# Optimization experiments

Hardware: AMD Instinct MI355X
Metric: run time of the kernel (lower is better)

## Reference

```python
import jax, jax.numpy as jnp
import numpy as np

EPS = 1e-5

def _layernorm(x, w, b):
    mu = jnp.mean(x, axis=-1, keepdims=True)
    var = jnp.var(x, axis=-1, keepdims=True)
    return (x - mu) * jax.lax.rsqrt(var + EPS) * w + b

def setup_inputs() -> dict:
    key = jax.random.key(0)
    ks = jax.random.split(key, 9)
    b, s, dim = 4, 4096, 2048
    m, n, dim_ctx = 8, 64, 1024
    heads, dim_head = 8, 64
    inner = heads * dim_head
    x = jax.random.normal(ks[0], (b, s, dim), dtype=jnp.float32)
    context = jax.random.normal(ks[1], (b, m, n, dim_ctx), dtype=jnp.float32)
    media_locations = jax.random.randint(ks[2], (b, s), 0, m, dtype=jnp.int64)
    scale = 0.02
    norm_w = jnp.ones((dim,), jnp.float32)
    norm_b = jnp.zeros((dim,), jnp.float32)
    normc_w = jnp.ones((dim_ctx,), jnp.float32)
    normc_b = jnp.zeros((dim_ctx,), jnp.float32)
    Wq = jax.random.normal(ks[3], (dim, inner), jnp.float32) * scale
    Wkv = jax.random.normal(ks[4], (dim_ctx, 2 * inner), jnp.float32) * scale
    Wout = jax.random.normal(ks[5], (inner, dim), jnp.float32) * scale
    return {"x": x, "context": context, "media_locations": media_locations,
            "norm_w": norm_w, "norm_b": norm_b, "normc_w": normc_w, "normc_b": normc_b,
            "Wq": Wq, "Wkv": Wkv, "Wout": Wout}

def reference(x, context, media_locations, norm_w, norm_b, normc_w, normc_b, Wq, Wkv, Wout):
    heads, dim_head = 8, 64
    b, m, n, dc = context.shape
    scale = dim_head ** -0.5
    xn = _layernorm(x, norm_w, norm_b)                       # [b,s,dim]
    ctx = _layernorm(context.reshape(b, m * n, dc), normc_w, normc_b)  # [b,mn,dc]
    q = xn @ Wq                                              # [b,s,inner]
    kv = ctx @ Wkv                                           # [b,mn,2*inner]
    k, v = jnp.split(kv, 2, axis=-1)
    def to_heads(t):
        return t.reshape(t.shape[0], t.shape[1], heads, dim_head).transpose(0, 2, 1, 3)
    q, k, v = to_heads(q), to_heads(k), to_heads(v)          # [b,h,*,d]
    sim = jnp.einsum('bhid,bhjd->bhij', q, k) * scale        # [b,h,s,mn]
    # image-causal mask: kv token j belongs to image j//n; query i may only
    # attend to image media_locations[b,i] (negative index => all masked)
    j_img = jnp.arange(m * n) // n                           # [mn]
    allowed = (media_locations[:, :, None] == j_img[None, None, :]) & (media_locations[:, :, None] >= 0)
    sim = jnp.where(allowed[:, None, :, :], sim, -jnp.inf)
    attn = jax.nn.softmax(sim, axis=-1)
    out = jnp.einsum('bhij,bhjd->bhid', attn, v)             # [b,h,s,d]
    out = out.transpose(0, 2, 1, 3).reshape(b, x.shape[1], heads * dim_head)
    return out @ Wout
```

## Files before the change

### kernel.cpp

```cpp
#include <hip/hip_runtime.h>

typedef unsigned short u16;
typedef unsigned int u32;
typedef __attribute__((ext_vector_type(8))) short short8;
typedef __attribute__((ext_vector_type(4))) short short4_t;
typedef __attribute__((ext_vector_type(4))) float f32x4;

__device__ __forceinline__ float bf2f(u16 u){ return __uint_as_float(((u32)u)<<16); }
__device__ __forceinline__ u16 f2bf(float f){ u32 x = __float_as_uint(f); return (u16)((x + 0x7FFFu + ((x>>16)&1u)) >> 16); }

#define OFF_FLAG   ((size_t)0)
#define OFF_COUNTS ((size_t)256)
#define OFF_LISTS  ((size_t)4096)
#define OFF_XN     ((size_t)(1<<20))
#define OFF_CTXN   (OFF_XN    + (size_t)67108864)
#define OFF_WQT    (OFF_CTXN  + (size_t)4194304)
#define OFF_WKVT   (OFF_WQT   + (size_t)2097152)
#define OFF_WOUTT  (OFF_WKVT  + (size_t)2097152)
#define OFF_Q      (OFF_WOUTT + (size_t)2097152)
#define OFF_KV     (OFF_Q     + (size_t)16777216)
#define OFF_ATTN   (OFF_KV    + (size_t)4194304)
#define OFF_VT     (OFF_ATTN  + (size_t)16777216)
#define WS_NEEDED  (OFF_VT    + (size_t)2097152)

__global__ __launch_bounds__(256) void prep_all(const float* __restrict__ x, const float* __restrict__ nw,
                                                const float* __restrict__ nb, u16* __restrict__ xn,
                                                const float* __restrict__ ctx, const float* __restrict__ ncw,
                                                const float* __restrict__ ncb, u16* __restrict__ ctxn,
                                                const float* __restrict__ Wq, const float* __restrict__ Wkv,
                                                const float* __restrict__ Wout, u16* __restrict__ WqT,
                                                u16* __restrict__ WkvT, u16* __restrict__ WoutT,
                                                const int* __restrict__ ml32, int* __restrict__ flag,
                                                int* __restrict__ counts){
  int id = blockIdx.x, tid = threadIdx.x;
  __shared__ float red[8];
  __shared__ float t[32][33];
  __shared__ int nz;
  if (id < 16384){
    constexpr int D = 2048, VEC = 8;
    const float* xr = x + (size_t)id*D;
    float v[VEC];
    #pragma unroll
    for (int i=0;i<VEC;i+=4){
      f32x4 f = *(const f32x4*)(xr + tid*VEC + i);
      v[i]=f[0]; v[i+1]=f[1]; v[i+2]=f[2]; v[i+3]=f[3];
    }
    float s=0.f, sq=0.f;
    #pragma unroll
    for (int i=0;i<VEC;++i){ s += v[i]; sq += v[i]*v[i]; }
    #pragma unroll
    for (int off=32;off;off>>=1){ s += __shfl_xor(s,off,64); sq += __shfl_xor(sq,off,64); }
    int lane = tid&63, wid = tid>>6;
    if (lane==0){ red[wid]=s; red[4+wid]=sq; }
    __syncthreads();
    s  = red[0]+red[1]+red[2]+red[3];
    sq = red[4]+red[5]+red[6]+red[7];
    float mu = s/(float)D;
    float var = sq/(float)D - mu*mu;
    float rs = rsqrtf(var + 1e-5f);
    u16 o[VEC];
    #pragma unroll
    for (int i=0;i<VEC;i+=4){
      f32x4 wv = *(const f32x4*)(nw + tid*VEC + i);
      f32x4 bv = *(const f32x4*)(nb + tid*VEC + i);
      #pragma unroll
      for (int u=0;u<4;++u) o[i+u] = f2bf((v[i+u]-mu)*rs*wv[u] + bv[u]);
    }
    *(short8*)(xn + (size_t)id*D + tid*8) = *(short8*)o;
  } else if (id < 18432){
    constexpr int D = 1024;
    int row = id - 16384;
    const float* xr = ctx + (size_t)row*D;
    f32x4 f = *(const f32x4*)(xr + tid*4);
    float s = f[0]+f[1]+f[2]+f[3];
    float sq = f[0]*f[0]+f[1]*f[1]+f[2]*f[2]+f[3]*f[3];
    #pragma unroll
    for (int off=32;off;off>>=1){ s += __shfl_xor(s,off,64); sq += __shfl_xor(sq,off,64); }
    int lane = tid&63, wid = tid>>6;
    if (lane==0){ red[wid]=s; red[4+wid]=sq; }
    __syncthreads();
    s  = red[0]+red[1]+red[2]+red[3];
    sq = red[4]+red[5]+red[6]+red[7];
    float mu = s/(float)D;
    float var = sq/(float)D - mu*mu;
    float rs = rsqrtf(var + 1e-5f);
    f32x4 wv = *(const f32x4*)(ncw + tid*4);
    f32x4 bv = *(const f32x4*)(ncb + tid*4);
    u16 o[4];
    #pragma unroll
    for (int u=0;u<4;++u) o[u] = f2bf((f[u]-mu)*rs*wv[u] + bv[u]);
    *(short4_t*)(ctxn + (size_t)row*D + tid*4) = *(short4_t*)o;
  } else if (id < 21504){
    int wid2 = id - 18432;
    const float* in; u16* out; int K, N, tile, tx_n;
    if (wid2 < 1024)      { in=Wq;   out=WqT;   K=2048; N=512;  tile=wid2;      tx_n=16; }
    else if (wid2 < 2048) { in=Wkv;  out=WkvT;  K=1024; N=1024; tile=wid2-1024; tx_n=32; }
    else                  { in=Wout; out=WoutT; K=512;  N=2048; tile=wid2-2048; tx_n=64; }
    int n0 = (tile % tx_n)*32, k0 = (tile / tx_n)*32;
    int tx = tid & 31, ty = tid >> 5;
    #pragma unroll
    for (int r=0;r<32;r+=8) t[ty+r][tx] = in[(size_t)(k0+ty+r)*N + n0+tx];
    __syncthreads();
    #pragma unroll
    for (int r=0;r<32;r+=8) out[(size_t)(n0+ty+r)*K + k0+tx] = f2bf(t[tx][ty+r]);
  } else {
    if (tid < 32) counts[tid] = 0;
    if (tid == 0) nz = 0;
    __syncthreads();
    if (tid < 128 && ml32[2*tid+1] != 0) atomicAdd(&nz, 1);
    __syncthreads();
    if (tid == 0) flag[0] = (nz == 0) ? 1 : 0;
  }
}

template<int MODE>
__device__ __forceinline__ void gemm_body(u16 (*lds)[2][128*32],
                                          const u16* __restrict__ A, const u16* __restrict__ B,
                                          void* __restrict__ Cv, int M, int N, int K, int wg0, int nwg,
                                          u16* __restrict__ vtp){
  int tid = threadIdx.x, lane = tid&63, wid = tid>>6;
  int nbn = N>>7;
  int wg = wg0;
  int cpx = nwg>>3;
  wg = (wg&7)*cpx + (wg>>3);
  int brow = wg/nbn, bcol = wg%nbn;

  auto stage = [&](int buf, int kt){
    #pragma unroll
    for (int i=0;i<2;++i){
      int cb = i*256 + wid*64;
      int c  = cb + lane;
      int row = c>>2, kc = c&3;
      const u16* ga = A + (size_t)(brow*128+row)*K + kt*32 + kc*8;
      __builtin_amdgcn_global_load_lds((const __attribute__((address_space(1))) u32*)ga,
          (__attribute__((address_space(3))) u32*)&lds[buf][0][cb*8], 16, 0, 0);
      const u16* gb = B + (size_t)(bcol*128+row)*K + kt*32 + kc*8;
      __builtin_amdgcn_global_load_lds((const __attribute__((address_space(1))) u32*)gb,
          (__attribute__((address_space(3))) u32*)&lds[buf][1][cb*8], 16, 0, 0);
    }
  };

  int wm = wid>>1, wn = wid&1;
  f32x4 acc[4][4] = {};
  int nkt = K>>5;
  stage(0,0);
  __syncthreads();
  for (int kt=0; kt<nkt; ++kt){
    int cur = kt&1;
    if (kt+1<nkt) stage(cur^1, kt+1);
    short8 af[4], bfr[4];
    int r = lane&15, kq = lane>>4;
    #pragma unroll
    for (int mi=0;mi<4;++mi) af[mi]  = *(const short8*)&lds[cur][0][(wm*64+mi*16+r)*32 + kq*8];
    #pragma unroll
    for (int ni=0;ni<4;++ni) bfr[ni] = *(const short8*)&lds[cur][1][(wn*64+ni*16+r)*32 + kq*8];
    #pragma unroll
    for (int mi=0;mi<4;++mi)
      #pragma unroll
      for (int ni=0;ni<4;++ni)
        acc[mi][ni] = __builtin_amdgcn_mfma_f32_16x16x32_bf16(af[mi], bfr[ni], acc[mi][ni], 0,0,0);
    __syncthreads();
  }
  int r4 = (lane>>4)*4, cc = lane&15;
  #pragma unroll
  for (int mi=0;mi<4;++mi){
    int rowb = brow*128 + wm*64 + mi*16 + r4;
    #pragma unroll
    for (int ni=0;ni<4;++ni){
      int col = bcol*128 + wn*64 + ni*16 + cc;
      #pragma unroll
      for (int rr=0;rr<4;++rr){
        int row = rowb + rr;
        float val = acc[mi][ni][rr];
        if (MODE==0)      ((float*)Cv)[(size_t)row*N+col] = val;
        else if (MODE==2) ((u16*)Cv)[(size_t)row*N+col] = f2bf(val*0.125f);
        else {
          if (col < 512)  ((u16*)Cv)[(size_t)row*N+col] = f2bf(val);
          else {
            int hv = (col-512)>>6, d = (col-512)&63;
            vtp[(size_t)((row>>6)*8 + hv)*4096 + d*64 + (row&63)] = f2bf(val);
          }
        }
      }
    }
  }
}

__global__ __launch_bounds__(256) void gemm_qkv(const u16* __restrict__ xn, const u16* __restrict__ WqT,
                                                u16* __restrict__ qbuf, const u16* __restrict__ ctxn,
                                                const u16* __restrict__ WkvT, u16* __restrict__ kvbuf,
                                                u16* __restrict__ vtbuf,
                                                const int* __restrict__ ml32, const int* __restrict__ flag,
                                                int* __restrict__ counts, int* __restrict__ lists){
  __shared__ __align__(16) u16 lds[2][2][128*32];
  __shared__ int lc[32], lbase[32];
  if (blockIdx.x < 512)      gemm_body<2>(lds, xn,   WqT,  qbuf,  16384, 512,  2048, blockIdx.x,     512, nullptr);
  else if (blockIdx.x < 640) gemm_body<3>(lds, ctxn, WkvT, kvbuf, 2048,  1024, 1024, blockIdx.x-512, 128, vtbuf);
  else {
    int bid = blockIdx.x - 640, tid = threadIdx.x;
    if (tid < 32) lc[tid] = 0;
    __syncthreads();
    int i = bid*256 + tid;
    int loc = flag[0] ? ml32[2*i] : ml32[i];
    int blk = (i>>12)*8 + loc;
    int lpos = atomicAdd(&lc[blk], 1);
    __syncthreads();
    if (tid < 32 && lc[tid] > 0) lbase[tid] = atomicAdd(&counts[tid], lc[tid]);
    __syncthreads();
    lists[blk*4096 + lbase[blk] + lpos] = i & 4095;
  }
}

__global__ __launch_bounds__(256) void gemm_out(const u16* __restrict__ A, const u16* __restrict__ B,
                                                float* __restrict__ C){
  __shared__ __align__(16) u16 lds[2][2][128*32];
  gemm_body<0>(lds, A, B, C, 16384, 2048, 512, blockIdx.x, gridDim.x, nullptr);
}

__global__ __launch_bounds__(512) void attn_mfma5(const u16* __restrict__ qb, const u16* __restrict__ kvb,
                                                  const u16* __restrict__ vt, u16* __restrict__ ob,
                                                  const int* __restrict__ counts, const int* __restrict__ lists){
  int bl = blockIdx.y, chunk = blockIdx.x;
  int cnt = counts[bl];
  int q0 = chunk*32;
  if (q0 >= cnt) return;
  int b = bl>>3, loc = bl&7;
  int tid = threadIdx.x, lane = tid&63, h = tid>>6;
  __shared__ u16 qs[32][520];
  int r = lane&15, g = lane>>4;

  const u16* kbase = kvb + (size_t)(b*512 + loc*64)*1024 + h*64;
  short8 kfr[4][2];
  #pragma unroll
  for (int nt=0;nt<4;++nt){
    const u16* krow = kbase + (size_t)(nt*16 + r)*1024;
    kfr[nt][0] = *(const short8*)(krow + g*8);
    kfr[nt][1] = *(const short8*)(krow + 32 + g*8);
  }
  const u16* vbase = vt + (size_t)(bl*8 + h)*4096;
  short8 vf[2][4];
  #pragma unroll
  for (int nt=0;nt<4;++nt){
    const u16* vrow = vbase + (size_t)(nt*16 + r)*64;
    vf[0][nt] = *(const short8*)(vrow + g*8);
    vf[1][nt] = *(const short8*)(vrow + 32 + g*8);
  }

  const u16* qbase = qb + (size_t)(b*4096)*512;
  #pragma unroll
  for (int p=0;p<4;++p){
    int c = p*512 + tid;
    int row = c>>6, cc = c&63;
    int qq = (q0 + row < cnt) ? lists[bl*4096 + q0 + row] : -1;
    if (qq >= 0)
      *(short8*)&qs[row][cc*8] = *(const short8*)(qbase + (size_t)qq*512 + cc*8);
  }
  __syncthreads();

  short8 qf[2][2];
  #pragma unroll
  for (int mt=0;mt<2;++mt){
    qf[mt][0] = *(const short8*)&qs[mt*16+r][h*64 + g*8];
    qf[mt][1] = *(const short8*)&qs[mt*16+r][h*64 + 32 + g*8];
  }

  f32x4 acc[2][4] = {};
  __builtin_amdgcn_s_setprio(1);
  #pragma unroll
  for (int mt=0;mt<2;++mt)
    #pragma unroll
    for (int nt=0;nt<4;++nt){
      acc[mt][nt] = __builtin_amdgcn_mfma_f32_16x16x32_bf16(qf[mt][0], kfr[nt][0], acc[mt][nt], 0,0,0);
      acc[mt][nt] = __builtin_amdgcn_mfma_f32_16x16x32_bf16(qf[mt][1], kfr[nt][1], acc[mt][nt], 0,0,0);
    }
  __builtin_amdgcn_s_setprio(0);

  #pragma unroll
  for (int mt=0;mt<2;++mt){
    #pragma unroll
    for (int rr=0;rr<4;++rr){
      float m = fmaxf(fmaxf(acc[mt][0][rr], acc[mt][1][rr]), fmaxf(acc[mt][2][rr], acc[mt][3][rr]));
      #pragma unroll
      for (int off=1;off<16;off<<=1) m = fmaxf(m, __shfl_xor(m, off));
      float e0 = __expf(acc[mt][0][rr]-m), e1 = __expf(acc[mt][1][rr]-m);
      float e2 = __expf(acc[mt][2][rr]-m), e3 = __expf(acc[mt][3][rr]-m);
      float sum = (e0+e1)+(e2+e3);
      #pragma unroll
      for (int off=1;off<16;off<<=1) sum += __shfl_xor(sum, off);
      float rs = 1.0f/sum;
      int row = mt*16 + g*4 + rr;
      qs[row][h*64 +  0 + r] = f2bf(e0*rs);
      qs[row][h*64 + 16 + r] = f2bf(e1*rs);
      qs[row][h*64 + 32 + r] = f2bf(e2*rs);
      qs[row][h*64 + 48 + r] = f2bf(e3*rs);
    }
  }

  f32x4 oacc[2][4] = {};
  #pragma unroll
  for (int mt=0;mt<2;++mt){
    short8 pa0 = *(const short8*)&qs[mt*16 + r][h*64 + g*8];
    short8 pa1 = *(const short8*)&qs[mt*16 + r][h*64 + 32 + g*8];
    __builtin_amdgcn_s_setprio(1);
    #pragma unroll
    for (int nt=0;nt<4;++nt){
      oacc[mt][nt] = __builtin_amdgcn_mfma_f32_16x16x32_bf16(pa0, vf[0][nt], oacc[mt][nt], 0,0,0);
      oacc[mt][nt] = __builtin_amdgcn_mfma_f32_16x16x32_bf16(pa1, vf[1][nt], oacc[mt][nt], 0,0,0);
    }
    __builtin_amdgcn_s_setprio(0);
  }

  #pragma unroll
  for (int mt=0;mt<2;++mt)
    #pragma unroll
    for (int rr=0;rr<4;++rr){
      int row = mt*16 + g*4 + rr;
      #pragma unroll
      for (int nt=0;nt<4;++nt)
        qs[row][h*64 + nt*16 + r] = f2bf(oacc[mt][nt][rr]);
    }
  __syncthreads();

  #pragma unroll
  for (int p=0;p<4;++p){
    int c = p*512 + tid;
    int row = c>>6, cc = c&63;
    int qq = (q0 + row < cnt) ? lists[bl*4096 + q0 + row] : -1;
    if (qq >= 0)
      *(short8*)(ob + ((size_t)(b*4096) + qq)*512 + cc*8) = *(const short8*)&qs[row][cc*8];
  }
}

extern "C" void kernel_launch(void* const* d_in, const int* in_sizes, int n_in,
                              void* d_out, int out_size, void* d_ws, size_t ws_size,
                              hipStream_t stream) {
  const float* x    = (const float*)d_in[0];
  const float* ctx  = (const float*)d_in[1];
  const int*   ml   = (const int*)d_in[2];
  const float* nw   = (const float*)d_in[3];
  const float* nb   = (const float*)d_in[4];
  const float* ncw  = (const float*)d_in[5];
  const float* ncb  = (const float*)d_in[6];
  const float* Wq   = (const float*)d_in[7];
  const float* Wkv  = (const float*)d_in[8];
  const float* Wout = (const float*)d_in[9];
  float* out = (float*)d_out;
  char* ws = (char*)d_ws;
  if (ws_size < WS_NEEDED) return;

  int* flag   = (int*)(ws + OFF_FLAG);
  int* counts = (int*)(ws + OFF_COUNTS);
  int* lists  = (int*)(ws + OFF_LISTS);
  u16* xn     = (u16*)(ws + OFF_XN);
  u16* ctxn   = (u16*)(ws + OFF_CTXN);
  u16* WqT    = (u16*)(ws + OFF_WQT);
  u16* WkvT   = (u16*)(ws + OFF_WKVT);
  u16* WoutT  = (u16*)(ws + OFF_WOUTT);
  u16* qbuf   = (u16*)(ws + OFF_Q);
  u16* kvbuf  = (u16*)(ws + OFF_KV);
  u16* attn_o = (u16*)(ws + OFF_ATTN);
  u16* vtbuf  = (u16*)(ws + OFF_VT);

  prep_all<<<21505,256,0,stream>>>(x, nw, nb, xn, ctx, ncw, ncb, ctxn,
                                   Wq, Wkv, Wout, WqT, WkvT, WoutT, ml, flag, counts);
  gemm_qkv<<<704,256,0,stream>>>(xn, WqT, qbuf, ctxn, WkvT, kvbuf, vtbuf, ml, flag, counts, lists);
  attn_mfma5<<<dim3(128,32),512,0,stream>>>(qbuf, kvbuf, vtbuf, attn_o, counts, lists);
  gemm_out<<<2048,256,0,stream>>>(attn_o, WoutT, out);
}
```

Measured before the change: 200.0 us.

## Replace output GEMM with 256x256-tile 8-wave kernel using direct global-to-LDS loads

The output projection GEMM moves from a generic 128x128-tile, 256-thread kernel to a dedicated 256x256-tile, 512-thread kernel. It stages A and B with global_load_lds into double-buffered LDS, interleaving the next tile's loads with MFMA phases and using set-priority around the MFMA bursts. It also swizzles block order across column groups. The intent is more data reuse per tile and overlap of memory with compute. The cost is higher register pressure from 32 accumulators per wave, more LDS use, and only 512 blocks, which gives fewer waves to hide latency.

```diff
diff --git a/kernel.cpp b/kernel.cpp
--- a/kernel.cpp
+++ b/kernel.cpp
@@ -172,8 +172,7 @@
       for (int rr=0;rr<4;++rr){
         int row = rowb + rr;
         float val = acc[mi][ni][rr];
-        if (MODE==0)      ((float*)Cv)[(size_t)row*N+col] = val;
-        else if (MODE==2) ((u16*)Cv)[(size_t)row*N+col] = f2bf(val*0.125f);
+        if (MODE==2) ((u16*)Cv)[(size_t)row*N+col] = f2bf(val*0.125f);
         else {
           if (col < 512)  ((u16*)Cv)[(size_t)row*N+col] = f2bf(val);
           else {
@@ -211,10 +210,100 @@
   }
 }
 
-__global__ __launch_bounds__(256) void gemm_out(const u16* __restrict__ A, const u16* __restrict__ B,
-                                                float* __restrict__ C){
-  __shared__ __align__(16) u16 lds[2][2][128*32];
-  gemm_body<0>(lds, A, B, C, 16384, 2048, 512, blockIdx.x, gridDim.x, nullptr);
+__global__ __launch_bounds__(512) void gemm_out8(const u16* __restrict__ A, const u16* __restrict__ B,
+                                                 float* __restrict__ C){
+  __shared__ __align__(16) u16 lA[2][16384];
+  __shared__ __align__(16) u16 lB[2][16384];
+  constexpr int N = 2048, K = 512, NKT = 8;
+  int tid = threadIdx.x, lane = tid&63;
+  int wid = tid>>6, wm = wid>>2, wn = wid&3;
+  int wg = blockIdx.x;
+  int cpx = 512>>3;
+  wg = (wg&7)*cpx + (wg>>3);
+  int brow = wg>>3, bcol = wg&7;
+
+  const u16* Abase = A + (size_t)(brow*256 + (tid>>3))*K + (tid&7)*8;
+  const u16* Bbase = B + (size_t)(bcol*256 + (tid>>3))*K + (tid&7)*8;
+
+  auto stage_pos = [&](int buf, int kt, int pos){
+    if (pos < 4){
+      const u16* g = Bbase + (size_t)(pos*64)*K + kt*64;
+      __builtin_amdgcn_global_load_lds((const __attribute__((address_space(1))) u32*)g,
+          (__attribute__((address_space(3))) u32*)&lB[buf][pos*4096 + tid*8], 16, 0, 0);
+    } else {
+      int ci = (pos==4) ? 0 : (pos==5) ? 2 : (pos==6) ? 1 : 3;
+      const u16* g = Abase + (size_t)(ci*64)*K + kt*64;
+      __builtin_amdgcn_global_load_lds((const __attribute__((address_space(1))) u32*)g,
+          (__attribute__((address_space(3))) u32*)&lA[buf][ci*4096 + tid*8], 16, 0, 0);
+    }
+  };
+
+  #pragma unroll
+  for (int pos=0; pos<8; ++pos) stage_pos(0, 0, pos);
+  asm volatile("s_waitcnt vmcnt(0)" ::: "memory");
+  __builtin_amdgcn_s_barrier();
+
+  f32x4 acc[8][4] = {};
+  int r = lane&15, kq = lane>>4;
+
+  for (int kt=0; kt<NKT; ++kt){
+    int cur = kt&1;
+    const u16* la = &lA[cur][0];
+    const u16* lb = &lB[cur][0];
+    bool has_next = (kt+1 < NKT);
+    short8 bf8[4][2];
+    #pragma unroll
+    for (int p=0;p<4;++p){
+      if (p==2){
+        if (has_next) asm volatile("s_waitcnt vmcnt(4)" ::: "memory");
+        else          asm volatile("s_waitcnt vmcnt(0)" ::: "memory");
+      }
+      if (has_next){
+        stage_pos(cur^1, kt+1, 2*p);
+        stage_pos(cur^1, kt+1, 2*p+1);
+      }
+      if (p==0){
+        #pragma unroll
+        for (int nt=0;nt<4;++nt)
+          #pragma unroll
+          for (int ks=0;ks<2;++ks)
+            bf8[nt][ks] = *(const short8*)&lb[(wn*64+nt*16+r)*64 + ks*32 + kq*8];
+      }
+      short8 af8[2][2];
+      #pragma unroll
+      for (int j=0;j<2;++j)
+        #pragma unroll
+        for (int ks=0;ks<2;++ks)
+          af8[j][ks] = *(const short8*)&la[(wm*128+(2*p+j)*16+r)*64 + ks*32 + kq*8];
+      __builtin_amdgcn_s_barrier();
+      __builtin_amdgcn_s_setprio(1);
+      #pragma unroll
+      for (int j=0;j<2;++j)
+        #pragma unroll
+        for (int nt=0;nt<4;++nt)
+          #pragma unroll
+          for (int ks=0;ks<2;++ks)
+            acc[2*p+j][nt] = __builtin_amdgcn_mfma_f32_16x16x32_bf16(af8[j][ks], bf8[nt][ks], acc[2*p+j][nt], 0,0,0);
+      __builtin_amdgcn_s_setprio(0);
+      __builtin_amdgcn_s_barrier();
+    }
+    if (has_next){
+      asm volatile("s_waitcnt lgkmcnt(0)" ::: "memory");
+      __builtin_amdgcn_sched_barrier(0);
+      asm volatile("s_waitcnt vmcnt(2)" ::: "memory");
+      __builtin_amdgcn_s_barrier();
+    }
+  }
+
+  int colb = bcol*256 + wn*64;
+  int rowb = brow*256 + wm*128;
+  #pragma unroll
+  for (int mt=0;mt<8;++mt)
+    #pragma unroll
+    for (int nt=0;nt<4;++nt)
+      #pragma unroll
+      for (int rr=0;rr<4;++rr)
+        C[(size_t)(rowb + mt*16 + kq*4 + rr)*N + colb + nt*16 + r] = acc[mt][nt][rr];
 }
 
 __global__ __launch_bounds__(512) void attn_mfma5(const u16* __restrict__ qb, const u16* __restrict__ kvb,
@@ -365,5 +454,5 @@
                                    Wq, Wkv, Wout, WqT, WkvT, WoutT, ml, flag, counts);
   gemm_qkv<<<704,256,0,stream>>>(xn, WqT, qbuf, ctxn, WkvT, kvbuf, vtbuf, ml, flag, counts, lists);
   attn_mfma5<<<dim3(128,32),512,0,stream>>>(qbuf, kvbuf, vtbuf, attn_o, counts, lists);
-  gemm_out<<<2048,256,0,stream>>>(attn_o, WoutT, out);
-}
+  gemm_out8<<<512,512,0,stream>>>(attn_o, WoutT, out);
+}
```

Measured after the change: 210.1 us. 5.0% more time.
